# Performance work log

Hardware: AMD Instinct MI355X
Metric: run time of the kernel (lower is better)

Reference implementation:

```python
import jax, jax.numpy as jnp
import numpy as np

WSIZES = (4, 8, 16)
IDX = (0, 1, 2, 1, 2, 0, 2, 0, 1)
BN_EPS = 1e-5


def _window_qv(el, ws):
    # el: [B, 2c, H, W] -> q, v each [(B*h*w), ws*ws, c]
    # matches rearrange 'b (qv c) (h dh) (w dw) -> qv (b h w) (dh dw) c'
    B, C2, H, W = el.shape
    c = C2 // 2
    h, w = H // ws, W // ws
    t = el.reshape(B, 2, c, h, ws, w, ws)
    t = t.transpose(1, 0, 3, 5, 4, 6, 2)  # qv, B, h, w, dh, dw, c
    t = t.reshape(2, B * h * w, ws * ws, c)
    return t[0], t[1]


def _match_batch(t, target_b):
    # replicate torch reshape-based window expansion/contraction
    b, s, c = t.shape
    if b < target_b:  # 'b (c wsize) h -> (b wsize) c h'
        ws = target_b // b
        return t.reshape(b, s // ws, ws, c).transpose(0, 2, 1, 3).reshape(b * ws, s // ws, c)
    if b > target_b:  # '(b wsize) c h -> b (c wsize) h'
        ws = b // target_b
        return t.reshape(target_b, ws, s, c).transpose(0, 2, 1, 3).reshape(target_b, s * ws, c)
    return t


def _unwindow(t, B, H, W, ws):
    # '(b h w) (dh dw) c -> b c (h dh) (w dw)'
    h, w = H // ws, W // ws
    c = t.shape[-1]
    return t.reshape(B, h, w, ws, ws, c).transpose(0, 5, 1, 3, 2, 4).reshape(B, c, H, W)


def _gmsa(x, w_in, b_in, bn_gamma, bn_beta, bn_mean, bn_var, w_out, b_out):
    B, C, H, W = x.shape
    # 1x1 conv + BatchNorm (eval-mode affine normalization)
    y = jnp.einsum('bchw,oc->bohw', x, w_in) + b_in[None, :, None, None]
    inv = bn_gamma / jnp.sqrt(bn_var + BN_EPS)
    y = y * inv[None, :, None, None] + (bn_beta - bn_mean * inv)[None, :, None, None]

    split = C * 2 // 3
    qs, vs = [], []
    for i, ws in enumerate(WSIZES):
        el = y[:, i * split:(i + 1) * split]
        el = jnp.roll(el, (-(ws // 2), -(ws // 2)), axis=(2, 3))  # shifts > 0
        q, v = _window_qv(el, ws)
        qs.append(q)
        vs.append(v)

    outs = []
    for i in range(0, 9, 3):
        q = qs[IDX[i]]
        k = _match_batch(qs[IDX[i + 1]], q.shape[0])
        v = _match_batch(vs[IDX[i + 2]], q.shape[0])
        atn = jax.nn.softmax(jnp.einsum('bic,bjc->bij', q, k), axis=-1)
        outs.append(jnp.einsum('bij,bjc->bic', atn, v))

    ys = []
    for i, ws in enumerate(WSIZES):
        yb = _unwindow(outs[i], B, H, W, ws)
        yb = jnp.roll(yb, (ws // 2, ws // 2), axis=(2, 3))
        ys.append(yb)
    y = jnp.concatenate(ys, axis=1)
    return jnp.einsum('bchw,oc->bohw', y, w_out) + b_out[None, :, None, None]


def setup_inputs() -> dict:
    key = jax.random.key(0)
    ks = jax.random.split(key, 9)
    C = 96
    return {
        'x': jax.random.normal(ks[0], (8, C, 256, 256), dtype=jnp.float32),
        'w_in': jax.random.normal(ks[1], (2 * C, C), dtype=jnp.float32) * (1.0 / np.sqrt(C)),
        'b_in': jax.random.normal(ks[2], (2 * C,), dtype=jnp.float32) * 0.02,
        'bn_gamma': jax.random.uniform(ks[3], (2 * C,), dtype=jnp.float32, minval=0.5, maxval=1.5),
        'bn_beta': jax.random.normal(ks[4], (2 * C,), dtype=jnp.float32) * 0.02,
        'bn_mean': jax.random.normal(ks[5], (2 * C,), dtype=jnp.float32) * 0.1,
        'bn_var': jax.random.uniform(ks[6], (2 * C,), dtype=jnp.float32, minval=0.5, maxval=1.5),
        'w_out': jax.random.normal(ks[7], (C, C), dtype=jnp.float32) * (1.0 / np.sqrt(C)),
        'b_out': jax.random.normal(ks[8], (C,), dtype=jnp.float32) * 0.02,
    }


def reference(x, w_in, b_in, bn_gamma, bn_beta, bn_mean, bn_var, w_out, b_out):
    return _gmsa(x, w_in, b_in, bn_gamma, bn_beta, bn_mean, bn_var, w_out, b_out)
```

## Files before the change

### kernel.cpp

```cpp
#include <hip/hip_runtime.h>


typedef _Float16 f16x8 __attribute__((ext_vector_type(8)));
typedef _Float16 f16x4 __attribute__((ext_vector_type(4)));
typedef _Float16 f16x2 __attribute__((ext_vector_type(2)));
typedef float    f32x4 __attribute__((ext_vector_type(4)));

__device__ inline float exp2_fast(float x) {
    float r; asm("v_exp_f32 %0, %1" : "=v"(r) : "v"(x)); return r;
}

__global__ __launch_bounds__(256) void k_prep(
    const float* __restrict__ w_in, const float* __restrict__ b_in,
    const float* __restrict__ gma, const float* __restrict__ bta,
    const float* __restrict__ mu,  const float* __restrict__ var,
    const float* __restrict__ w_out,
    _Float16* __restrict__ wf, float* __restrict__ bs, _Float16* __restrict__ wo)
{
    const int t = threadIdx.x;
    if (t < 192) {
        const float qs = ((t & 63) < 32) ? 1.2011224087864498f : 1.0f;
        float iv = gma[t] * rsqrtf(var[t] + 1e-5f);
        float s  = iv * qs;
        bs[t] = (b_in[t]*iv + bta[t] - mu[t]*iv) * qs;
        #pragma unroll
        for (int c4 = 0; c4 < 96; c4 += 4) {
            float4 w = *reinterpret_cast<const float4*>(w_in + t*96 + c4);
            f16x4 h;
            h[0]=(_Float16)(w.x*s); h[1]=(_Float16)(w.y*s);
            h[2]=(_Float16)(w.z*s); h[3]=(_Float16)(w.w*s);
            *reinterpret_cast<f16x4*>(wf + t*96 + c4) = h;
        }
    }
    if (t < 96) {
        #pragma unroll
        for (int c4 = 0; c4 < 96; c4 += 4) {
            float4 w = *reinterpret_cast<const float4*>(w_out + t*96 + c4);
            f16x4 h;
            h[0]=(_Float16)w.x; h[1]=(_Float16)w.y;
            h[2]=(_Float16)w.z; h[3]=(_Float16)w.w;
            *reinterpret_cast<f16x4*>(wo + t*96 + c4) = h;
        }
    }
}

__global__ __launch_bounds__(256) void k_conv_in(
    const float* __restrict__ x, const _Float16* __restrict__ wf,
    const float* __restrict__ bs,
    _Float16* __restrict__ q0, _Float16* __restrict__ v0,
    _Float16* __restrict__ q1, _Float16* __restrict__ v1,
    _Float16* __restrict__ q2, _Float16* __restrict__ v2)
{
    __shared__ float xs[32*132];
    const int t  = threadIdx.x;
    const int wv = t >> 6, ln = t & 63;
    const int lo = ln & 15, hi = ln >> 4;
    const int oh = wv >> 1, ph = wv & 1;

    const int pixbase = blockIdx.x * 128;
    const int b   = pixbase >> 16;
    const int rem = pixbase & 65535;
    const int hh  = rem >> 8;
    const int ww0 = rem & 255;

    const int r0 = t >> 5;
    const int q4 = (t & 31) * 4;
    const float* xb = x + (size_t)b*96*65536 + rem + q4;

    float4 RA0, RA1, RA2, RA3, RB0, RB1, RB2, RB3;

#define STAGE_LOAD(Ra,Rb,Rc,Rd,c0) { \
    Ra = *reinterpret_cast<const float4*>(xb + (size_t)(c0 + r0     )*65536); \
    Rb = *reinterpret_cast<const float4*>(xb + (size_t)(c0 + r0 +  8)*65536); \
    Rc = *reinterpret_cast<const float4*>(xb + (size_t)(c0 + r0 + 16)*65536); \
    Rd = *reinterpret_cast<const float4*>(xb + (size_t)(c0 + r0 + 24)*65536); }
#define STAGE_WRITE(Ra,Rb,Rc,Rd) { \
    *reinterpret_cast<float4*>(&xs[(r0     )*132 + q4]) = Ra; \
    *reinterpret_cast<float4*>(&xs[(r0 +  8)*132 + q4]) = Rb; \
    *reinterpret_cast<float4*>(&xs[(r0 + 16)*132 + q4]) = Rc; \
    *reinterpret_cast<float4*>(&xs[(r0 + 24)*132 + q4]) = Rd; }

    STAGE_LOAD(RA0, RA1, RA2, RA3, 0);

    f16x8 af[6][3];
    const _Float16* wrow0 = wf + (size_t)(oh*96 + lo)*96 + hi*8;
    #pragma unroll
    for (int rf = 0; rf < 6; ++rf)
        #pragma unroll
        for (int ks = 0; ks < 3; ++ks)
            af[rf][ks] = *reinterpret_cast<const f16x8*>(wrow0 + rf*16*96 + ks*32);

    f32x4 acc[6][4];
    #pragma unroll
    for (int rf = 0; rf < 6; ++rf)
        #pragma unroll
        for (int cf = 0; cf < 4; ++cf) acc[rf][cf] = f32x4{0.f,0.f,0.f,0.f};

#define COMPUTE(j) { \
    _Pragma("unroll") for (int cf = 0; cf < 4; ++cf) { \
        const float* bp = &xs[hi*8*132 + ph*64 + cf*16 + lo]; \
        f16x8 bfv; \
        _Pragma("unroll") for (int e = 0; e < 8; ++e) bfv[e] = (_Float16)bp[e*132]; \
        _Pragma("unroll") for (int rf = 0; rf < 6; ++rf) \
            acc[rf][cf] = __builtin_amdgcn_mfma_f32_16x16x32_f16( \
                              af[rf][j], bfv, acc[rf][cf], 0,0,0); } }

    STAGE_WRITE(RA0, RA1, RA2, RA3);
    STAGE_LOAD(RB0, RB1, RB2, RB3, 32);
    __syncthreads();
    COMPUTE(0);
    __syncthreads();
    STAGE_WRITE(RB0, RB1, RB2, RB3);
    STAGE_LOAD(RA0, RA1, RA2, RA3, 64);
    __syncthreads();
    COMPUTE(1);
    __syncthreads();
    STAGE_WRITE(RA0, RA1, RA2, RA3);
    __syncthreads();
    COMPUTE(2);

    int ro[3][4];
    #pragma unroll
    for (int i = 0; i < 3; ++i) {
        const int lg = 2 + i;
        const int ws = 1 << lg;
        const int sft = ws >> 1;
        const int nblk = 256 >> lg;
        int h  = (hh - sft) & 255;
        int nbrow = (b*nblk + (h >> lg))*nblk;
        int hr = h & (ws-1);
        #pragma unroll
        for (int cf = 0; cf < 4; ++cf) {
            int w = (ww0 + ph*64 + cf*16 + lo - sft) & 255;
            ro[i][cf] = (nbrow + (w >> lg))*(ws*ws) + hr*ws + (w & (ws-1));
        }
    }
    #pragma unroll
    for (int rf = 0; rf < 6; ++rf) {
        const int base = oh*96 + rf*16;
        const int o0i  = base + hi*4;
        const int sc   = base >> 6;
        const bool isv = (base & 32) != 0;
        const int c32  = o0i & 31;
        float4 bi = *reinterpret_cast<const float4*>(bs + o0i);
        _Float16* tb = (sc == 0) ? (isv ? v0 : q0)
                     : (sc == 1) ? (isv ? v1 : q1)
                                 : (isv ? v2 : q2);
        #pragma unroll
        for (int cf = 0; cf < 4; ++cf) {
            f16x4 hv;
            hv[0] = (_Float16)(acc[rf][cf][0] + bi.x);
            hv[1] = (_Float16)(acc[rf][cf][1] + bi.y);
            hv[2] = (_Float16)(acc[rf][cf][2] + bi.z);
            hv[3] = (_Float16)(acc[rf][cf][3] + bi.w);
            *reinterpret_cast<f16x4*>(tb + (size_t)ro[sc][cf]*32 + c32) = hv;
        }
    }
#undef STAGE_LOAD
#undef STAGE_WRITE
#undef COMPUTE
}

template<int GROUP>
__global__ __launch_bounds__(256) void k_attn(
    const _Float16* __restrict__ Q, const _Float16* __restrict__ Ks,
    const _Float16* Vs, _Float16* O)
{
    constexpr int S   = (GROUP==0) ? 16 : (GROUP==1) ? 64 : 256;
    constexpr int GB  = 256 / S;
    constexpr int KT  = (S < 32) ? 16 : 32;
    constexpr int NT  = S / KT;
    constexpr int CBS = KT / 16;

    __shared__ uint4    Kl[4*256];
    __shared__ _Float16 Vt[32*264 + 8];
    __shared__ _Float16 Pl[4][64*40];

    const int t = threadIdx.x;
    {
        const int g = t / S, j = t % S;
        const int bq = blockIdx.x * GB + g;
        int krow, vrow;
        if constexpr (GROUP == 0) {
            krow = (bq >> 2)*64  + (j << 2) + (bq & 3);
            vrow = (bq >> 4)*256 + (j << 4) + (bq & 15);
        } else if constexpr (GROUP == 1) {
            krow = (bq >> 2)*256 + (j << 2) + (bq & 3);
            vrow = ((bq << 2) + (j & 3))*16 + (j >> 2);
        } else {
            krow = ((bq << 4) + (j & 15))*16 + (j >> 4);
            vrow = ((bq << 2) + (j & 3))*64 + (j >> 2);
        }
        const uint4* ks = reinterpret_cast<const uint4*>(Ks + (size_t)krow*32);
        uint4 ka = ks[0], kb = ks[1], kc = ks[2], kd = ks[3];
        Kl[0*256 + t] = ka; Kl[1*256 + t] = kb;
        Kl[2*256 + t] = kc; Kl[3*256 + t] = kd;
        union { uint4 u4[4]; _Float16 h[32]; } vb;
        const uint4* vs = reinterpret_cast<const uint4*>(Vs + (size_t)vrow*32);
        vb.u4[0] = vs[0]; vb.u4[1] = vs[1]; vb.u4[2] = vs[2]; vb.u4[3] = vs[3];
        #pragma unroll
        for (int d = 0; d < 32; ++d) Vt[d*264 + t] = vb.h[d];
        Vt[(t >> 3)*264 + 256 + (t & 7)] = (_Float16)0.f;
        if (t < 8) Vt[32*264 + t] = (_Float16)0.f;
    }
    const int wv = t >> 6, ln = t & 63;
    const int lo = ln & 15, hi = ln >> 4;
    _Float16* Pw = Pl[wv];
    if constexpr (S == 16) {
        uint* pw32 = reinterpret_cast<uint*>(Pw);
        #pragma unroll
        for (int k2 = 0; k2 < 8; ++k2) {
            int idx = ln + k2*64;
            pw32[(idx >> 3)*20 + 8 + (idx & 7)] = 0u;
        }
    }
    __syncthreads();

    const int rowbase = blockIdx.x*256 + wv*64;
    f16x8 qf[4];
    #pragma unroll
    for (int rb = 0; rb < 4; ++rb) {
        uint4 qv = *reinterpret_cast<const uint4*>(
            Q + ((size_t)(rowbase + rb*16 + lo))*32 + hi*8);
        qf[rb] = __builtin_bit_cast(f16x8, qv);
    }

    f32x4 ofr[4][2];
    float m[4], ls[4];
    #pragma unroll
    for (int rb = 0; rb < 4; ++rb) {
        m[rb] = -1e30f; ls[rb] = 0.f;
        ofr[rb][0] = f32x4{0.f,0.f,0.f,0.f};
        ofr[rb][1] = f32x4{0.f,0.f,0.f,0.f};
    }
    const f32x4 zf = f32x4{0.f,0.f,0.f,0.f};

    for (int tt = 0; tt < NT; ++tt) {
        f32x4 sf[4][CBS];
        if constexpr (S == 16) {
            #pragma unroll
            for (int rb = 0; rb < 4; ++rb) {
                int key = wv*64 + rb*16 + lo;
                f16x8 bk = __builtin_bit_cast(f16x8, Kl[hi*256 + key]);
                sf[rb][0] = __builtin_amdgcn_mfma_f32_16x16x32_f16(bk, qf[rb], zf, 0,0,0);
            }
        } else {
            f16x8 bk[CBS];
            const int wb = (S == 64) ? wv*64 : 0;
            #pragma unroll
            for (int cb = 0; cb < CBS; ++cb) {
                int key = wb + tt*KT + cb*16 + lo;
                bk[cb] = __builtin_bit_cast(f16x8, Kl[hi*256 + key]);
            }
            #pragma unroll
            for (int rb = 0; rb < 4; ++rb)
                #pragma unroll
                for (int cb = 0; cb < CBS; ++cb)
                    sf[rb][cb] = __builtin_amdgcn_mfma_f32_16x16x32_f16(bk[cb], qf[rb], zf, 0,0,0);
        }

        #pragma unroll
        for (int rb = 0; rb < 4; ++rb) {
            float tm = sf[rb][0][0];
            #pragma unroll
            for (int cb = 0; cb < CBS; ++cb)
                #pragma unroll
                for (int r = 0; r < 4; ++r)
                    if (cb | r) tm = fmaxf(tm, sf[rb][cb][r]);
            tm = fmaxf(tm, __shfl_xor(tm, 16));
            tm = fmaxf(tm, __shfl_xor(tm, 32));
            float mn = fmaxf(m[rb], tm);
            float sc = exp2_fast(m[rb] - mn);
            m[rb] = mn;
            float ps = 0.f;
            #pragma unroll
            for (int cb = 0; cb < CBS; ++cb) {
                float p0 = exp2_fast(sf[rb][cb][0] - mn);
                float p1 = exp2_fast(sf[rb][cb][1] - mn);
                float p2 = exp2_fast(sf[rb][cb][2] - mn);
                float p3 = exp2_fast(sf[rb][cb][3] - mn);
                ps += (p0+p1)+(p2+p3);
                f16x2 w01; w01[0] = (_Float16)p0; w01[1] = (_Float16)p1;
                f16x2 w23; w23[0] = (_Float16)p2; w23[1] = (_Float16)p3;
                _Float16* pp = Pw + (rb*16 + lo)*40 + cb*16 + hi*4;
                *reinterpret_cast<f16x2*>(pp)     = w01;
                *reinterpret_cast<f16x2*>(pp + 2) = w23;
            }
            ls[rb] = ls[rb]*sc + ps;
            float s0 = __shfl(sc, hi*4 + 0);
            float s1 = __shfl(sc, hi*4 + 1);
            float s2 = __shfl(sc, hi*4 + 2);
            float s3 = __shfl(sc, hi*4 + 3);
            ofr[rb][0][0]*=s0; ofr[rb][0][1]*=s1; ofr[rb][0][2]*=s2; ofr[rb][0][3]*=s3;
            ofr[rb][1][0]*=s0; ofr[rb][1][1]*=s1; ofr[rb][1][2]*=s2; ofr[rb][1][3]*=s3;
        }

        #pragma unroll
        for (int rb = 0; rb < 4; ++rb) {
            f16x8 pa = *reinterpret_cast<const f16x8*>(Pw + (rb*16 + lo)*40 + hi*8);
            const int wb = (S == 16) ? wv*64 + rb*16 : (S == 64) ? wv*64 : 0;
            const int key0 = wb + tt*KT + hi*8;
            #pragma unroll
            for (int dcb = 0; dcb < 2; ++dcb) {
                f16x8 bv = *reinterpret_cast<const f16x8*>(Vt + (dcb*16 + lo)*264 + key0);
                ofr[rb][dcb] = __builtin_amdgcn_mfma_f32_16x16x32_f16(pa, bv, ofr[rb][dcb], 0,0,0);
            }
        }
    }

    #pragma unroll
    for (int rb = 0; rb < 4; ++rb) {
        float v = ls[rb];
        v += __shfl_xor(v, 16);
        v += __shfl_xor(v, 32);
        float linv = 1.f / v;
        float l0 = __shfl(linv, hi*4 + 0);
        float l1 = __shfl(linv, hi*4 + 1);
        float l2 = __shfl(linv, hi*4 + 2);
        float l3 = __shfl(linv, hi*4 + 3);
        #pragma unroll
        for (int dcb = 0; dcb < 2; ++dcb) {
            float lr[4] = {l0, l1, l2, l3};
            #pragma unroll
            for (int r = 0; r < 4; ++r) {
                float ov = ofr[rb][dcb][r] * lr[r];
                int row = rowbase + rb*16 + hi*4 + r;
                O[(size_t)row*32 + dcb*16 + lo] = (_Float16)ov;
            }
        }
    }
}

__global__ __launch_bounds__(256) void k_conv_out(
    const _Float16* __restrict__ o0, const _Float16* __restrict__ o1,
    const _Float16* __restrict__ o2, const _Float16* __restrict__ wo,
    const float* __restrict__ b_out, float* __restrict__ out)
{
    constexpr int YS = 104;
    __shared__ _Float16 yt[256*YS];
    const int t  = threadIdx.x;
    const int wv = t >> 6, ln = t & 63;
    const int lo = ln & 15, hi = ln >> 4;
    const int bid = (int)blockIdx.x;
    const int swz = (bid & 7)*256 + (bid >> 3);
    const int b = swz >> 8;
    const int h = swz & 255;

    #pragma unroll
    for (int i = 0; i < 3; ++i) {
        const int lg = 2 + i;
        const int ws = 1 << lg;
        const int sft = ws >> 1;
        const int nblk = 256 >> lg;
        int hh = (h - sft) & 255;
        int w  = (t - sft) & 255;
        int nb = (b*nblk + (hh >> lg))*nblk + (w >> lg);
        int roff = nb*(ws*ws) + (hh & (ws-1))*ws + (w & (ws-1));
        const uint4* src = reinterpret_cast<const uint4*>(
            (i==0 ? o0 : i==1 ? o1 : o2) + (size_t)roff*32);
        uint4 r0 = src[0], r1 = src[1], r2 = src[2], r3 = src[3];
        uint4* dst = reinterpret_cast<uint4*>(&yt[t*YS + i*32]);
        dst[0] = r0; dst[1] = r1; dst[2] = r2; dst[3] = r3;
    }

    f16x8 af[6][3];
    #pragma unroll
    for (int rf = 0; rf < 6; ++rf)
        #pragma unroll
        for (int ks = 0; ks < 3; ++ks)
            af[rf][ks] = *reinterpret_cast<const f16x8*>(
                wo + (rf*16 + lo)*96 + ks*32 + hi*8);
    __syncthreads();

    f32x4 acc[6][4];
    #pragma unroll
    for (int rf = 0; rf < 6; ++rf)
        #pragma unroll
        for (int cf = 0; cf < 4; ++cf) acc[rf][cf] = f32x4{0.f,0.f,0.f,0.f};

    #pragma unroll
    for (int cf = 0; cf < 4; ++cf) {
        const int px = wv*64 + cf*16 + lo;
        #pragma unroll
        for (int ks = 0; ks < 3; ++ks) {
            f16x8 bfv = *reinterpret_cast<const f16x8*>(&yt[px*YS + ks*32 + hi*8]);
            #pragma unroll
            for (int rf = 0; rf < 6; ++rf)
                acc[rf][cf] = __builtin_amdgcn_mfma_f32_16x16x32_f16(
                                  af[rf][ks], bfv, acc[rf][cf], 0,0,0);
        }
    }

    const size_t obase = (size_t)b*96*65536 + (size_t)h*256;
    #pragma unroll
    for (int rf = 0; rf < 6; ++rf) {
        const int oo = rf*16 + hi*4;
        float4 bi = *reinterpret_cast<const float4*>(b_out + oo);
        #pragma unroll
        for (int cf = 0; cf < 4; ++cf) {
            const int px = wv*64 + cf*16 + lo;
            out[obase + (size_t)(oo+0)*65536 + px] = acc[rf][cf][0] + bi.x;
            out[obase + (size_t)(oo+1)*65536 + px] = acc[rf][cf][1] + bi.y;
            out[obase + (size_t)(oo+2)*65536 + px] = acc[rf][cf][2] + bi.z;
            out[obase + (size_t)(oo+3)*65536 + px] = acc[rf][cf][3] + bi.w;
        }
    }
}

extern "C" void kernel_launch(void* const* d_in, const int* in_sizes, int n_in,
                              void* d_out, int out_size, void* d_ws, size_t ws_size,
                              hipStream_t stream)
{
    const float* x     = (const float*)d_in[0];
    const float* w_in  = (const float*)d_in[1];
    const float* b_in  = (const float*)d_in[2];
    const float* gma   = (const float*)d_in[3];
    const float* bta   = (const float*)d_in[4];
    const float* mu    = (const float*)d_in[5];
    const float* var   = (const float*)d_in[6];
    const float* w_out = (const float*)d_in[7];
    const float* b_out = (const float*)d_in[8];
    float* out = (float*)d_out;

    _Float16* W = (_Float16*)d_ws;
    const size_t M = 16777216;
    _Float16 *q0 = W,       *v0 = W +   M, *q1 = W + 2*M,
             *v1 = W + 3*M, *q2 = W + 4*M, *v2 = W + 5*M;
    _Float16* wf = W + 6*M;
    float*    bs = (float*)(W + 6*M + 18432);
    _Float16* wo = W + 6*M + 18432 + 384;

    k_prep<<<1, 256, 0, stream>>>(w_in, b_in, gma, bta, mu, var, w_out, wf, bs, wo);
    k_conv_in<<<4096, 256, 0, stream>>>(x, wf, bs, q0, v0, q1, v1, q2, v2);
    k_attn<0><<<2048, 256, 0, stream>>>(q0, q1, v2, v2);
    k_attn<1><<<2048, 256, 0, stream>>>(q1, q2, v0, v0);
    k_attn<2><<<2048, 256, 0, stream>>>(q2, q0, v1, v1);
    k_conv_out<<<2048, 256, 0, stream>>>(v2, v0, v1, wo, b_out, out);
}
```

Before: 287.7 us.

## Stage conv input as packed fp16 in double-buffered LDS and merge attention launches

k_conv_in now converts x to fp16 pairs with cvt_pkrtz before writing to shared memory. It uses two buffers, which halves LDS traffic and removes the per-element fp32->fp16 conversion in the MFMA inner loop, and cuts the number of barriers. The three k_attn launches are merged into one 6144-block kernel that dispatches by block index, removing two launch boundaries and their tail drains. The softmax P conversion also switches to packed round-toward-zero conversion, which slightly changes rounding behaviour.

```diff
diff --git a/kernel.cpp b/kernel.cpp
--- a/kernel.cpp
+++ b/kernel.cpp
@@ -8,6 +8,9 @@
 
 __device__ inline float exp2_fast(float x) {
     float r; asm("v_exp_f32 %0, %1" : "=v"(r) : "v"(x)); return r;
+}
+__device__ inline unsigned pkrtz(float a, float b) {
+    return __builtin_bit_cast(unsigned, __builtin_amdgcn_cvt_pkrtz(a, b));
 }
 
 __global__ __launch_bounds__(256) void k_prep(
@@ -51,7 +54,7 @@
     _Float16* __restrict__ q1, _Float16* __restrict__ v1,
     _Float16* __restrict__ q2, _Float16* __restrict__ v2)
 {
-    __shared__ float xs[32*132];
+    __shared__ unsigned xs2[2][16*132];
     const int t  = threadIdx.x;
     const int wv = t >> 6, ln = t & 63;
     const int lo = ln & 15, hi = ln >> 4;
@@ -64,23 +67,34 @@
     const int ww0 = rem & 255;
 
     const int r0 = t >> 5;
-    const int q4 = (t & 31) * 4;
+    const int q4 = (t & 31) << 2;
     const float* xb = x + (size_t)b*96*65536 + rem + q4;
 
-    float4 RA0, RA1, RA2, RA3, RB0, RB1, RB2, RB3;
-
-#define STAGE_LOAD(Ra,Rb,Rc,Rd,c0) { \
-    Ra = *reinterpret_cast<const float4*>(xb + (size_t)(c0 + r0     )*65536); \
-    Rb = *reinterpret_cast<const float4*>(xb + (size_t)(c0 + r0 +  8)*65536); \
-    Rc = *reinterpret_cast<const float4*>(xb + (size_t)(c0 + r0 + 16)*65536); \
-    Rd = *reinterpret_cast<const float4*>(xb + (size_t)(c0 + r0 + 24)*65536); }
-#define STAGE_WRITE(Ra,Rb,Rc,Rd) { \
-    *reinterpret_cast<float4*>(&xs[(r0     )*132 + q4]) = Ra; \
-    *reinterpret_cast<float4*>(&xs[(r0 +  8)*132 + q4]) = Rb; \
-    *reinterpret_cast<float4*>(&xs[(r0 + 16)*132 + q4]) = Rc; \
-    *reinterpret_cast<float4*>(&xs[(r0 + 24)*132 + q4]) = Rd; }
-
-    STAGE_LOAD(RA0, RA1, RA2, RA3, 0);
+    float4 L0, L1, L2, L3;
+
+#define CLOAD(c0) { \
+    L0 = *reinterpret_cast<const float4*>(xb + (size_t)(c0 + 2*r0     )*65536); \
+    L1 = *reinterpret_cast<const float4*>(xb + (size_t)(c0 + 2*r0 +  1)*65536); \
+    L2 = *reinterpret_cast<const float4*>(xb + (size_t)(c0 + 2*r0 + 16)*65536); \
+    L3 = *reinterpret_cast<const float4*>(xb + (size_t)(c0 + 2*r0 + 17)*65536); }
+#define CWRITE(bf) { \
+    uint4 u0, u1; \
+    u0.x = pkrtz(L0.x, L1.x); u0.y = pkrtz(L0.y, L1.y); \
+    u0.z = pkrtz(L0.z, L1.z); u0.w = pkrtz(L0.w, L1.w); \
+    u1.x = pkrtz(L2.x, L3.x); u1.y = pkrtz(L2.y, L3.y); \
+    u1.z = pkrtz(L2.z, L3.z); u1.w = pkrtz(L2.w, L3.w); \
+    *reinterpret_cast<uint4*>(&xs2[bf][ r0     *132 + q4]) = u0; \
+    *reinterpret_cast<uint4*>(&xs2[bf][(r0 + 8)*132 + q4]) = u1; }
+#define CCOMP(bf, ks) { \
+    _Pragma("unroll") for (int cf = 0; cf < 4; ++cf) { \
+        const unsigned* bp = &xs2[bf][hi*4*132 + ph*64 + cf*16 + lo]; \
+        uint4 u; u.x = bp[0]; u.y = bp[132]; u.z = bp[264]; u.w = bp[396]; \
+        f16x8 bfv = __builtin_bit_cast(f16x8, u); \
+        _Pragma("unroll") for (int rf = 0; rf < 6; ++rf) \
+            acc[rf][cf] = __builtin_amdgcn_mfma_f32_16x16x32_f16( \
+                              af[rf][ks], bfv, acc[rf][cf], 0,0,0); } }
+
+    CLOAD(0);
 
     f16x8 af[6][3];
     const _Float16* wrow0 = wf + (size_t)(oh*96 + lo)*96 + hi*8;
@@ -96,28 +110,17 @@
         #pragma unroll
         for (int cf = 0; cf < 4; ++cf) acc[rf][cf] = f32x4{0.f,0.f,0.f,0.f};
 
-#define COMPUTE(j) { \
-    _Pragma("unroll") for (int cf = 0; cf < 4; ++cf) { \
-        const float* bp = &xs[hi*8*132 + ph*64 + cf*16 + lo]; \
-        f16x8 bfv; \
-        _Pragma("unroll") for (int e = 0; e < 8; ++e) bfv[e] = (_Float16)bp[e*132]; \
-        _Pragma("unroll") for (int rf = 0; rf < 6; ++rf) \
-            acc[rf][cf] = __builtin_amdgcn_mfma_f32_16x16x32_f16( \
-                              af[rf][j], bfv, acc[rf][cf], 0,0,0); } }
-
-    STAGE_WRITE(RA0, RA1, RA2, RA3);
-    STAGE_LOAD(RB0, RB1, RB2, RB3, 32);
+    CWRITE(0);
     __syncthreads();
-    COMPUTE(0);
+    CLOAD(32);
+    CCOMP(0, 0);
+    CWRITE(1);
     __syncthreads();
-    STAGE_WRITE(RB0, RB1, RB2, RB3);
-    STAGE_LOAD(RA0, RA1, RA2, RA3, 64);
+    CLOAD(64);
+    CCOMP(1, 1);
+    CWRITE(0);
     __syncthreads();
-    COMPUTE(1);
-    __syncthreads();
-    STAGE_WRITE(RA0, RA1, RA2, RA3);
-    __syncthreads();
-    COMPUTE(2);
+    CCOMP(0, 2);
 
     int ro[3][4];
     #pragma unroll
@@ -156,13 +159,14 @@
             *reinterpret_cast<f16x4*>(tb + (size_t)ro[sc][cf]*32 + c32) = hv;
         }
     }
-#undef STAGE_LOAD
-#undef STAGE_WRITE
-#undef COMPUTE
+#undef CLOAD
+#undef CWRITE
+#undef CCOMP
 }
 
 template<int GROUP>
-__global__ __launch_bounds__(256) void k_attn(
+__device__ __forceinline__ void attn_body(
+    int bid, uint4* Kl, _Float16* Vt, _Float16* Pl,
     const _Float16* __restrict__ Q, const _Float16* __restrict__ Ks,
     const _Float16* Vs, _Float16* O)
 {
@@ -172,14 +176,10 @@
     constexpr int NT  = S / KT;
     constexpr int CBS = KT / 16;
 
-    __shared__ uint4    Kl[4*256];
-    __shared__ _Float16 Vt[32*264 + 8];
-    __shared__ _Float16 Pl[4][64*40];
-
     const int t = threadIdx.x;
     {
         const int g = t / S, j = t % S;
-        const int bq = blockIdx.x * GB + g;
+        const int bq = bid * GB + g;
         int krow, vrow;
         if constexpr (GROUP == 0) {
             krow = (bq >> 2)*64  + (j << 2) + (bq & 3);
@@ -205,7 +205,7 @@
     }
     const int wv = t >> 6, ln = t & 63;
     const int lo = ln & 15, hi = ln >> 4;
-    _Float16* Pw = Pl[wv];
+    _Float16* Pw = Pl + wv*(64*40);
     if constexpr (S == 16) {
         uint* pw32 = reinterpret_cast<uint*>(Pw);
         #pragma unroll
@@ -216,7 +216,7 @@
     }
     __syncthreads();
 
-    const int rowbase = blockIdx.x*256 + wv*64;
+    const int rowbase = bid*256 + wv*64;
     f16x8 qf[4];
     #pragma unroll
     for (int rb = 0; rb < 4; ++rb) {
@@ -280,11 +280,11 @@
                 float p2 = exp2_fast(sf[rb][cb][2] - mn);
                 float p3 = exp2_fast(sf[rb][cb][3] - mn);
                 ps += (p0+p1)+(p2+p3);
-                f16x2 w01; w01[0] = (_Float16)p0; w01[1] = (_Float16)p1;
-                f16x2 w23; w23[0] = (_Float16)p2; w23[1] = (_Float16)p3;
+                unsigned w01 = pkrtz(p0, p1);
+                unsigned w23 = pkrtz(p2, p3);
                 _Float16* pp = Pw + (rb*16 + lo)*40 + cb*16 + hi*4;
-                *reinterpret_cast<f16x2*>(pp)     = w01;
-                *reinterpret_cast<f16x2*>(pp + 2) = w23;
+                *reinterpret_cast<unsigned*>(pp)     = w01;
+                *reinterpret_cast<unsigned*>(pp + 2) = w23;
             }
             ls[rb] = ls[rb]*sc + ps;
             float s0 = __shfl(sc, hi*4 + 0);
@@ -329,6 +329,24 @@
             }
         }
     }
+}
+
+__global__ __launch_bounds__(256) void k_attn_all(
+    const _Float16* __restrict__ q0, const _Float16* __restrict__ v0,
+    const _Float16* __restrict__ q1, const _Float16* __restrict__ v1,
+    const _Float16* __restrict__ q2, const _Float16* __restrict__ v2)
+{
+    __shared__ __align__(16) char smem[16384 + 16912 + 20480];
+    uint4*    Kl = reinterpret_cast<uint4*>(smem);
+    _Float16* Vt = reinterpret_cast<_Float16*>(smem + 16384);
+    _Float16* Pl = reinterpret_cast<_Float16*>(smem + 16384 + 16912);
+    const int bid = (int)blockIdx.x;
+    if (bid < 2048)
+        attn_body<0>(bid, Kl, Vt, Pl, q0, q1, v2, const_cast<_Float16*>(v2));
+    else if (bid < 4096)
+        attn_body<1>(bid - 2048, Kl, Vt, Pl, q1, q2, v0, const_cast<_Float16*>(v0));
+    else
+        attn_body<2>(bid - 4096, Kl, Vt, Pl, q2, q0, v1, const_cast<_Float16*>(v1));
 }
 
 __global__ __launch_bounds__(256) void k_conv_out(
@@ -432,8 +450,6 @@
 
     k_prep<<<1, 256, 0, stream>>>(w_in, b_in, gma, bta, mu, var, w_out, wf, bs, wo);
     k_conv_in<<<4096, 256, 0, stream>>>(x, wf, bs, q0, v0, q1, v1, q2, v2);
-    k_attn<0><<<2048, 256, 0, stream>>>(q0, q1, v2, v2);
-    k_attn<1><<<2048, 256, 0, stream>>>(q1, q2, v0, v0);
-    k_attn<2><<<2048, 256, 0, stream>>>(q2, q0, v1, v1);
+    k_attn_all<<<6144, 256, 0, stream>>>(q0, v0, q1, v1, q2, v2);
     k_conv_out<<<2048, 256, 0, stream>>>(v2, v0, v1, wo, b_out, out);
 }
```

Measured after the change: 276.8 us. -3.8%, faster.
